# Performance work log

Measured on AMD Instinct MI355X. Metric: run time of the kernel, lower is better.

Reference implementation:

```python
import jax, jax.numpy as jnp
import numpy as np

D = 64; T = 128; B = 64; R = 20; SEE = 10; H = 4; C = 4
N = 300000; P = 4000; K = 256


def setup_inputs() -> dict:
    key = jax.random.key(0)
    ks = jax.random.split(key, 24)
    g = lambda k, s: jax.random.normal(k, s, dtype=jnp.float32) * 0.05
    return {
        "prob_id": jax.random.randint(ks[0], (T, B), 0, P),
        "skills": jax.random.randint(ks[1], (T, B, C), 0, K),
        "response": jax.random.randint(ks[2], (T, B), 0, 2),
        "bg_index": jax.random.randint(ks[3], (T, B, R), 0, N),
        "mem_prob_ids": jax.random.randint(ks[4], (N,), 0, P),
        "mem_resp": jax.random.randint(ks[5], (N,), 0, 2),
        "mem_concepts": jax.random.randint(ks[6], (N, C), 0, K),
        "states_mem": g(ks[7], (N, D)),
        "concept_emb": g(ks[8], (K - 1, D)),
        "prob_emb": g(ks[9], (P - 1, D)),
        "W_pred": g(ks[10], (9 * D, 1)), "b_pred": jnp.zeros((1,), jnp.float32),
        "W_ih": g(ks[11], (4 * D, 3 * D)), "W_hh": g(ks[12], (D, 3 * D)),
        "b_ih": jnp.zeros((3 * D,), jnp.float32), "b_hh": jnp.zeros((3 * D,), jnp.float32),
        "W_batch": g(ks[13], (H, 3 * D, D)), "b_batch": jnp.zeros((H, D), jnp.float32),
        "W_bg": g(ks[14], (H, 3 * D, D)), "b_bg": jnp.zeros((H, D), jnp.float32),
        "W_bgint": g(ks[15], (6 * D, 6 * D)), "b_bgint": jnp.zeros((6 * D,), jnp.float32),
        "W_hisint": g(ks[16], (2 * D, 6 * D)), "b_hisint": jnp.zeros((6 * D,), jnp.float32),
        "W_inmap": g(ks[17], (10 * D, 4 * D)), "b_inmap": jnp.zeros((4 * D,), jnp.float32),
        "dir_w": g(ks[18], (2, 1)), "heads_map": g(ks[19], (H, 1)),
    }


def _forward(floats, ints):
    (states_mem, concept_emb, prob_emb, W_pred, b_pred, W_ih, W_hh, b_ih, b_hh,
     W_batch, b_batch, W_bg, b_bg, W_bgint, b_bgint, W_hisint, b_hisint,
     W_inmap, b_inmap, dir_w, heads_map) = floats
    prob_id, skills, response, bg_index, mem_prob_ids, mem_resp, mem_concepts = ints
    f32 = states_mem.dtype
    # embedding tables with zero row 0 (padding id)
    prob_cat = jnp.concatenate([jnp.zeros((1, D), f32), prob_emb], axis=0)
    conc_cat = jnp.concatenate([jnp.zeros((1, D), f32), concept_emb], axis=0)

    def prob_rep(pid, sk):
        pr = prob_cat[pid]                                     # [..., D]
        fsum = jnp.sum((sk != 0).astype(f32), axis=-1)
        div = jnp.where(fsum == 0, 1.0, fsum)[..., None]
        mean = jnp.sum(conc_cat[sk], axis=-2) / div            # masked-mean concept emb
        return jnp.concatenate([mean, pr], axis=-1)            # [..., 2D]

    dw = jax.nn.softmax(dir_w, axis=0)                          # [2,1]
    hm = heads_map[:, 0]                                        # [H]

    def step(carry, xt):
        h, h_buf, resp_buf, v_buf, t = carry
        pid, sk, resp, bgi = xt
        respf = resp.astype(f32)
        v = prob_rep(pid, sk)                                   # [B,2D]
        hidden_v = jnp.concatenate([h, v], axis=-1)             # [B,3D]
        bgi = bgi[:, :SEE]                                      # keep first see_ref refs
        bg_h = states_mem[bgi]                                  # [B,S,D] irregular gather
        bg_v = prob_rep(mem_prob_ids[bgi], mem_concepts[bgi])   # [B,S,2D]
        bg_r = mem_resp[bgi].astype(f32)[..., None]             # [B,S,1]
        all_hv = jnp.concatenate([bg_h, bg_v], axis=-1)         # [B,S,3D]
        bg_ctx = jnp.concatenate([all_hv * bg_r, all_hv * (1.0 - bg_r)], axis=-1)  # [B,S,6D]
        # multi-head attention over retrieved background states
        q = jnp.einsum('bk,hkd->bhd', hidden_v, W_batch) + b_batch[None]
        kk = jnp.einsum('bsk,hkd->bhsd', all_hv, W_bg) + b_bg[None, :, None, :]
        att = jax.nn.softmax(jnp.einsum('bhd,bhsd->bhs', q, kk) / np.sqrt(3.0 * D), axis=-1)
        heads = jnp.einsum('bhs,bsk->bhk', att, bg_ctx)          # [B,H,6D]
        bg_atts = jnp.einsum('bhk,h->bk', heads, hm)             # [B,6D]
        # attention over own history (positions 0..t valid)
        rb = resp_buf.astype(f32)[..., None]                     # [B,T+1,1]
        hr_cat = jnp.concatenate([h_buf * rb, h_buf * (1.0 - rb)], axis=-1)  # [B,T+1,2D]
        sc = jnp.einsum('bk,btk->bt', v, v_buf) / np.sqrt(2.0 * D)
        sc = jnp.where(jnp.arange(T + 1)[None, :] <= t, sc, -1e9)
        his_atts = jnp.einsum('bt,btk->bk', jax.nn.softmax(sc, axis=-1), hr_cat)  # [B,2D]
        peer = (bg_atts @ W_bgint + b_bgint) * dw[0, 0] + (his_atts @ W_hisint + b_hisint) * dw[1, 0]
        prob = (jnp.concatenate([peer, v, h], axis=-1) @ W_pred + b_pred)[:, 0]
        v_resp = jnp.concatenate([v * respf[:, None], v * (1.0 - respf[:, None])], axis=-1)
        gru_in = jnp.concatenate([peer, v_resp], axis=-1) @ W_inmap + b_inmap  # [B,4D]
        # GRU cell (torch GRUCell convention)
        gx = gru_in @ W_ih + b_ih
        gh = h @ W_hh + b_hh
        xr, xz, xn = jnp.split(gx, 3, axis=-1)
        hr, hz, hn = jnp.split(gh, 3, axis=-1)
        r = jax.nn.sigmoid(xr + hr)
        z = jax.nn.sigmoid(xz + hz)
        n = jnp.tanh(xn + r * hn)
        new_h = (1.0 - z) * n + z * h
        h_buf = h_buf.at[:, t + 1].set(new_h)
        resp_buf = resp_buf.at[:, t + 1].set(resp.astype(resp_buf.dtype))
        v_buf = v_buf.at[:, t + 1].set(v)
        return (new_h, h_buf, resp_buf, v_buf, t + 1), prob

    init = (jnp.zeros((B, D), f32), jnp.zeros((B, T + 1, D), f32),
            jnp.zeros((B, T + 1), jnp.int32), jnp.zeros((B, T + 1, 2 * D), f32),
            jnp.int32(0))
    xs = (prob_id, skills, response.astype(jnp.int32), bg_index)
    _, probs = jax.lax.scan(step, init, xs)                      # [T,B]
    return probs.T.reshape(-1)                                   # concat over batch, seq_num=T


def reference(prob_id, skills, response, bg_index, mem_prob_ids, mem_resp, mem_concepts,
              states_mem, concept_emb, prob_emb, W_pred, b_pred, W_ih, W_hh, b_ih, b_hh,
              W_batch, b_batch, W_bg, b_bg, W_bgint, b_bgint, W_hisint, b_hisint,
              W_inmap, b_inmap, dir_w, heads_map):
    floats = (states_mem, concept_emb, prob_emb, W_pred, b_pred, W_ih, W_hh, b_ih, b_hh,
              W_batch, b_batch, W_bg, b_bg, W_bgint, b_bgint, W_hisint, b_hisint,
              W_inmap, b_inmap, dir_w, heads_map)
    ints = (prob_id, skills, response, bg_index, mem_prob_ids, mem_resp, mem_concepts)
    return _forward(floats, ints)
```

## Files before the change

### kernel.cpp

```cpp
#include <hip/hip_runtime.h>
#include <hip/hip_bf16.h>

#define TT 128
#define BB 64
#define NITEM (TT*BB*SEE)
#define SEE 10
typedef __attribute__((ext_vector_type(8))) short short8;
typedef __attribute__((ext_vector_type(4))) float floatx4;

static __device__ __forceinline__ float wave_sum(float v) {
  v += __shfl_xor(v, 32); v += __shfl_xor(v, 16); v += __shfl_xor(v, 8);
  v += __shfl_xor(v, 4);  v += __shfl_xor(v, 2);  v += __shfl_xor(v, 1);
  return v;
}
static __device__ __forceinline__ float wave_max(float v) {
  v = fmaxf(v, __shfl_xor(v, 32)); v = fmaxf(v, __shfl_xor(v, 16)); v = fmaxf(v, __shfl_xor(v, 8));
  v = fmaxf(v, __shfl_xor(v, 4));  v = fmaxf(v, __shfl_xor(v, 2));  v = fmaxf(v, __shfl_xor(v, 1));
  return v;
}
static __device__ __forceinline__ unsigned short f2bf(float x) {
  __hip_bfloat16 h = __float2bfloat16(x);
  return *reinterpret_cast<unsigned short*>(&h);
}
static __device__ __forceinline__ float bf2f(unsigned short u) {
  unsigned v = ((unsigned)u) << 16;
  return __builtin_bit_cast(float, v);
}
static __device__ __forceinline__ unsigned int pack2(float lo, float hi) {
  return (unsigned int)f2bf(lo) | ((unsigned int)f2bf(hi) << 16);
}
static __device__ __forceinline__ void ldsbar() {
  asm volatile("s_waitcnt lgkmcnt(0)" ::: "memory");
  __builtin_amdgcn_s_barrier();
  asm volatile("" ::: "memory");
}

__global__ void build_v(const int* __restrict__ prob_id, const int* __restrict__ skills,
                        const float* __restrict__ concept_emb, const float* __restrict__ prob_emb,
                        float* __restrict__ V, float* __restrict__ VT) {
  int tb = blockIdx.x; int t = tb >> 6, b = tb & 63; int d = threadIdx.x;
  int pid = prob_id[tb];
  float pr = pid ? prob_emb[(pid - 1) * 64 + d] : 0.0f;
  int cnt = 0; float sum = 0.0f;
#pragma unroll
  for (int c = 0; c < 4; ++c) {
    int sk = skills[tb * 4 + c];
    if (sk) { ++cnt; sum += concept_emb[(sk - 1) * 64 + d]; }
  }
  float mean = sum / (float)(cnt ? cnt : 1);
  V[tb * 128 + d] = mean;
  V[tb * 128 + 64 + d] = pr;
  VT[b * 16384 + d * 128 + t] = mean;
  VT[b * 16384 + (64 + d) * 128 + t] = pr;
}

__global__ __launch_bounds__(256) void gather_ahv(
    const int* __restrict__ bg_index, const int* __restrict__ mem_prob_ids,
    const int* __restrict__ mem_concepts, const float* __restrict__ states_mem,
    const float* __restrict__ concept_emb, const float* __restrict__ prob_emb,
    unsigned short* __restrict__ AHV) {
  int gid = blockIdx.x * 256 + threadIdx.x;
  int item = gid / 96, c2 = gid - 96 * item; int d = 2 * c2;
  int t = item / 640; int rem = item - t * 640; int b = rem / 10; int s = rem - b * 10;
  int g = bg_index[(t * 64 + b) * 20 + s];
  float v0, v1;
  if (d < 64) {
    float2 sv = *(const float2*)&states_mem[g * 64 + d];
    v0 = sv.x; v1 = sv.y;
  } else if (d < 128) {
    int dd = d - 64; float s0 = 0.f, s1 = 0.f; int cnt = 0;
#pragma unroll
    for (int c = 0; c < 4; ++c) {
      int sk = mem_concepts[g * 4 + c];
      if (sk) { ++cnt; float2 e = *(const float2*)&concept_emb[(sk - 1) * 64 + dd]; s0 += e.x; s1 += e.y; }
    }
    float inv = 1.0f / (float)(cnt ? cnt : 1);
    v0 = s0 * inv; v1 = s1 * inv;
  } else {
    int dd = d - 128; int pid = mem_prob_ids[g];
    if (pid) { float2 pv = *(const float2*)&prob_emb[(pid - 1) * 64 + dd]; v0 = pv.x; v1 = pv.y; }
    else { v0 = 0.f; v1 = 0.f; }
  }
  *(unsigned int*)&AHV[(size_t)item * 192 + d] = pack2(v0, v1);
}

__global__ __launch_bounds__(256) void gemm_f32(
    const float* __restrict__ A, const float* __restrict__ B, float* __restrict__ C,
    const float* __restrict__ bias, int M, int N, int K,
    int lda, int ldb, int ldc, long sA, long sB, long sC, float scale) {
  __shared__ __align__(16) float As[64 * 36];
  __shared__ __align__(16) float Bs[32 * 64];
  const float* Ab = A + (long)blockIdx.z * sA;
  const float* Bb = B + (long)blockIdx.z * sB;
  float* Cb = C + (long)blockIdx.z * sC;
  int m0 = blockIdx.y * 64, n0 = blockIdx.x * 64;
  int tid = threadIdx.x;
  int ti = tid & 15, tj = tid >> 4;
  float acc[4][4] = {};
  for (int kc = 0; kc < K; kc += 32) {
#pragma unroll
    for (int p = 0; p < 2; ++p) {
      int q = tid + 256 * p;
      int row = q >> 3, kq = q & 7;
      *(float4*)&As[row * 36 + 4 * kq] = *(const float4*)&Ab[(size_t)(m0 + row) * lda + kc + 4 * kq];
    }
#pragma unroll
    for (int p = 0; p < 2; ++p) {
      int q = tid + 256 * p;
      int k = q >> 4, nq = q & 15;
      *(float4*)&Bs[k * 64 + 4 * nq] = *(const float4*)&Bb[(size_t)(kc + k) * ldb + n0 + 4 * nq];
    }
    __syncthreads();
#pragma unroll
    for (int k4 = 0; k4 < 8; ++k4) {
      float4 av[4], bv[4];
#pragma unroll
      for (int m = 0; m < 4; ++m) av[m] = *(const float4*)&As[(ti + 16 * m) * 36 + 4 * k4];
#pragma unroll
      for (int kk = 0; kk < 4; ++kk) bv[kk] = *(const float4*)&Bs[(4 * k4 + kk) * 64 + 4 * tj];
#pragma unroll
      for (int m = 0; m < 4; ++m) {
        const float* ap = (const float*)&av[m];
#pragma unroll
        for (int kk = 0; kk < 4; ++kk) {
          float a = ap[kk];
          acc[m][0] += a * bv[kk].x; acc[m][1] += a * bv[kk].y;
          acc[m][2] += a * bv[kk].z; acc[m][3] += a * bv[kk].w;
        }
      }
    }
    __syncthreads();
  }
  float4 bq = make_float4(0.f, 0.f, 0.f, 0.f);
  if (bias) bq = *(const float4*)&bias[n0 + 4 * tj];
#pragma unroll
  for (int m = 0; m < 4; ++m) {
    int row = m0 + ti + 16 * m;
    float4 o;
    o.x = acc[m][0] * scale + bq.x; o.y = acc[m][1] * scale + bq.y;
    o.z = acc[m][2] * scale + bq.z; o.w = acc[m][3] * scale + bq.w;
    *(float4*)&Cb[(size_t)row * ldc + n0 + 4 * tj] = o;
  }
}

__global__ __launch_bounds__(256) void k_small(
    const float* __restrict__ W_batch, const float* __restrict__ W_bg, const float* __restrict__ b_bg,
    const float* __restrict__ W_bgint, const float* __restrict__ b_bgint,
    const float* __restrict__ W_hisint, const float* __restrict__ b_hisint,
    const float* __restrict__ W_ih, const float* __restrict__ b_ih, const float* __restrict__ b_inmap,
    const float* __restrict__ W_pred, const float* __restrict__ b_pred, const float* __restrict__ dir_w,
    const float* __restrict__ b_batch,
    const float* __restrict__ M12, unsigned short* __restrict__ B1T, float* __restrict__ Hmix,
    float* __restrict__ WgT, float* __restrict__ BQG, float* __restrict__ biasQG,
    float* __restrict__ c4, float* __restrict__ cgx, float* __restrict__ uh,
    float* __restrict__ bgp, float* __restrict__ c0, float* __restrict__ dwv) {
  int idx = blockIdx.x * 256 + threadIdx.x;
  const int R0 = 49152, R1 = 86016, R2 = 122880, R3 = 147456, R4 = 196608,
            R5 = 229376, R6 = 278528, R7 = 278784, R8 = 278976, R9 = 279104,
            R10 = 279488, R11 = 279489, R12 = 279491, R13 = 280131;
  if (idx < R0) {
    int k = idx >> 8, n = idx & 255; int h = n >> 6, i = n & 63;
    float s = 0.f;
    for (int d = 0; d < 64; ++d) s += W_bg[h * 12288 + k * 64 + d] * W_batch[h * 12288 + i * 64 + d];
    B1T[n * 192 + k] = f2bf(s);
  } else if (idx < R1) {
    int r = idx - R0; int k = r / 192, c = r - k * 192;
    float s = 0.f;
    for (int j = 0; j < 384; ++j) s += W_bgint[k * 384 + j] * M12[j * 192 + c];
    B1T[(256 + c) * 192 + k] = f2bf(s);
  } else if (idx < R2) {
    int r = idx - R1; int k = r / 192, c = r - k * 192;
    float s = 0.f;
    for (int j = 0; j < 384; ++j) s += W_bgint[(192 + k) * 384 + j] * M12[j * 192 + c];
    B1T[(448 + c) * 192 + k] = f2bf(s);
  } else if (idx < R3) {
    int r = idx - R2; int i = r / 192, c = r - i * 192;
    float s = 0.f;
    for (int j = 0; j < 384; ++j) s += W_hisint[i * 384 + j] * M12[j * 192 + c];
    Hmix[i * 192 + c] = s;
  } else if (idx < R4) {
    int r = idx - R3; int h = r / 12288; int rem = r - h * 12288; int d = rem / 192, k = rem - d * 192;
    WgT[r] = W_bg[h * 12288 + k * 64 + d];
  } else if (idx < R5) {
    int r = idx - R4; int i = r >> 8, n = r & 255; int h = n >> 6, d = n & 63;
    BQG[i * 640 + n] = W_batch[h * 12288 + (64 + i) * 64 + d];
  } else if (idx < R6) {
    int r = idx - R5; int i = r / 384, c = r - i * 384;
    BQG[i * 640 + 256 + c] = (c < 192) ? M12[(384 + i) * 192 + c] : M12[(512 + i) * 192 + (c - 192)];
  } else if (idx < R7) {
    int n = idx - R6; int h = n >> 6, i = n & 63;
    float s = 0.f;
    for (int d = 0; d < 64; ++d) s += W_batch[h * 12288 + i * 64 + d] * b_bg[h * 64 + d];
    c4[n] = s;
  } else if (idx < R8) {
    int c = idx - R7;
    float e0 = __expf(dir_w[0]), e1 = __expf(dir_w[1]);
    float dw0 = e0 / (e0 + e1), dw1 = e1 / (e0 + e1);
    float s = b_ih[c];
    for (int i = 0; i < 256; ++i) s += b_inmap[i] * W_ih[i * 192 + c];
    for (int k = 0; k < 384; ++k) s += (dw0 * b_bgint[k] + dw1 * b_hisint[k]) * M12[k * 192 + c];
    cgx[c] = s;
  } else if (idx < R9) {
    int i = idx - R8;
    float s = 0.f;
    for (int j = 0; j < 384; ++j) s += W_hisint[i * 384 + j] * W_pred[j];
    uh[i] = s;
  } else if (idx < R10) {
    int k = idx - R9;
    float s = 0.f;
    for (int j = 0; j < 384; ++j) s += W_bgint[k * 384 + j] * W_pred[j];
    bgp[k] = s;
  } else if (idx < R11) {
    float e0 = __expf(dir_w[0]), e1 = __expf(dir_w[1]);
    float dw0 = e0 / (e0 + e1), dw1 = e1 / (e0 + e1);
    float s = b_pred[0];
    for (int k = 0; k < 384; ++k) s += (dw0 * b_bgint[k] + dw1 * b_hisint[k]) * W_pred[k];
    c0[0] = s;
  } else if (idx < R12) {
    float e0 = __expf(dir_w[0]), e1 = __expf(dir_w[1]);
    dwv[idx - R11] = (idx == R11) ? e0 / (e0 + e1) : e1 / (e0 + e1);
  } else if (idx < R13) {
    int i = idx - R12;
    biasQG[i] = (i < 256) ? b_batch[i] : 0.f;
  }
}

#define APAD 200
#define BPAD 40
__global__ __launch_bounds__(256) void big_gemm(
    const int* __restrict__ bg_index, const int* __restrict__ mem_resp,
    const unsigned short* __restrict__ AHV, const unsigned short* __restrict__ B1T,
    const float* __restrict__ c4, unsigned short* __restrict__ P4s16, float* __restrict__ Cg) {
  __shared__ unsigned short As[128 * APAD];
  __shared__ unsigned short Bs[128 * BPAD];
  __shared__ int rf_l[128];
  int mt = blockIdx.x;
  int tid = threadIdx.x;
  int lane = tid & 63, wv = tid >> 6;
  if (tid < 128) {
    int item = mt * 128 + tid;
    int t = item / 640; int rem = item - t * 640; int b = rem / 10; int s = rem - b * 10;
    int g = bg_index[(t * 64 + b) * 20 + s];
    rf_l[tid] = mem_resp[g];
  }
  for (int i = tid; i < 128 * 24; i += 256) {
    int row = i / 24, c = i - 24 * row;
    *(float4*)&As[row * APAD + c * 8] = *(const float4*)&AHV[(size_t)(mt * 128 + row) * 192 + c * 8];
  }
  int l15 = lane & 15, q = lane >> 4;
  int mh = (wv & 1) * 64, nh = (wv >> 1) * 64;
  const float invs192 = 0.07216878364870323f;
  for (int nt = 0; nt < 5; ++nt) {
    int n0 = nt * 128;
    floatx4 acc[4][4];
#pragma unroll
    for (int mi = 0; mi < 4; ++mi)
#pragma unroll
      for (int ni = 0; ni < 4; ++ni)
#pragma unroll
        for (int r = 0; r < 4; ++r) acc[mi][ni][r] = 0.f;
    for (int kc = 0; kc < 6; ++kc) {
      __syncthreads();
#pragma unroll
      for (int u = 0; u < 2; ++u) {
        int un = tid * 2 + u;
        int n = un >> 2, kk = (un & 3) * 8;
        *(float4*)&Bs[n * BPAD + kk] = *(const float4*)&B1T[(size_t)(n0 + n) * 192 + kc * 32 + kk];
      }
      __syncthreads();
      short8 a[4], bfr[4];
#pragma unroll
      for (int mi = 0; mi < 4; ++mi)
        a[mi] = *reinterpret_cast<const short8*>(&As[(mh + mi * 16 + l15) * APAD + kc * 32 + q * 8]);
#pragma unroll
      for (int ni = 0; ni < 4; ++ni)
        bfr[ni] = *reinterpret_cast<const short8*>(&Bs[(nh + ni * 16 + l15) * BPAD + q * 8]);
#pragma unroll
      for (int mi = 0; mi < 4; ++mi)
#pragma unroll
        for (int ni = 0; ni < 4; ++ni)
          acc[mi][ni] = __builtin_amdgcn_mfma_f32_16x16x32_bf16(a[mi], bfr[ni], acc[mi][ni], 0, 0, 0);
    }
    float c4v[4];
    if (n0 + nh < 256) {
#pragma unroll
      for (int ni = 0; ni < 4; ++ni) c4v[ni] = c4[n0 + nh + ni * 16 + l15];
    }
#pragma unroll
    for (int mi = 0; mi < 4; ++mi) {
#pragma unroll
      for (int r = 0; r < 4; ++r) {
        int row = mh + mi * 16 + q * 4 + r;
        int item = mt * 128 + row;
        int rf = rf_l[row];
#pragma unroll
        for (int ni = 0; ni < 4; ++ni) {
          int coln = n0 + nh + ni * 16 + l15;
          float o = acc[mi][ni][r];
          if (coln < 256) {
            P4s16[(size_t)item * 256 + coln] = f2bf((o + c4v[ni]) * invs192);
          } else if (coln < 448) {
            if (rf) Cg[(size_t)item * 192 + (coln - 256)] = o;
          } else {
            if (!rf) Cg[(size_t)item * 192 + (coln - 448)] = o;
          }
        }
      }
    }
  }
}

__global__ __launch_bounds__(256) void k5(
    const int* __restrict__ bg_index, const int* __restrict__ mem_resp,
    const unsigned short* __restrict__ AHV, const float* __restrict__ RQ,
    const float* __restrict__ QVG, const float* __restrict__ b_bg,
    const float* __restrict__ bgp, const float* __restrict__ V,
    const float* __restrict__ W_pred, const float* __restrict__ c0,
    float* __restrict__ SQVb, float* __restrict__ cbp, float* __restrict__ PROBC) {
  int tb = blockIdx.x;
  int tid = threadIdx.x;
  int lane = tid & 63, wv = tid >> 6;
  __shared__ float ahv[10 * 196];
  __shared__ float rql[4 * 196];
  __shared__ float bgpl[384];
  __shared__ int rf_s[10];
  __shared__ float cqb[4];
  if (tid < 10) { int g = bg_index[tb * 20 + tid]; rf_s[tid] = mem_resp[g]; }
  for (int i = tid; i < 384; i += 256) bgpl[i] = bgp[i];
  for (int i = tid; i < 768; i += 256) { int h = i / 192, c = i - h * 192; rql[h * 196 + c] = RQ[(size_t)tb * 768 + i]; }
  {
    const unsigned short* AH = &AHV[(size_t)tb * 10 * 192];
    for (int i = tid; i < 1920; i += 256) {
      int s = i / 192, c = i - 192 * s;
      ahv[s * 196 + c] = bf2f(AH[s * 192 + c]);
    }
  }
  if (tid < 4) {
    float s = 0.f;
    for (int d = 0; d < 64; ++d) s += QVG[(size_t)tb * 640 + tid * 64 + d] * b_bg[tid * 64 + d];
    cqb[tid] = s;
  }
  __syncthreads();
  const float invs192 = 0.07216878364870323f;
  for (int q = 0; q < 10; ++q) {
    float v = ahv[q * 196 + lane] * rql[wv * 196 + lane]
            + ahv[q * 196 + 64 + lane] * rql[wv * 196 + 64 + lane]
            + ahv[q * 196 + 128 + lane] * rql[wv * 196 + 128 + lane];
    v = wave_sum(v);
    if (lane == 0) SQVb[tb * 40 + wv * 10 + q] = (v + cqb[wv]) * invs192;
  }
  if (wv == 0) {
    for (int q = 0; q < 10; ++q) {
      int off = rf_s[q] ? 0 : 192;
      float v = ahv[q * 196 + lane] * bgpl[off + lane]
              + ahv[q * 196 + 64 + lane] * bgpl[off + 64 + lane]
              + ahv[q * 196 + 128 + lane] * bgpl[off + 128 + lane];
      v = wave_sum(v);
      if (lane == 0) cbp[tb * 10 + q] = v;
    }
  }
  if (wv == 1) {
    float v = V[tb * 128 + lane] * W_pred[384 + lane] + V[tb * 128 + 64 + lane] * W_pred[448 + lane];
    v = wave_sum(v);
    if (lane == 0) PROBC[tb] = v + c0[0];
  }
}

__global__ __launch_bounds__(64) void prep_pw(const float* S, const int* response,
                                              float* PW, float* PR) {
  int bt = blockIdx.x; int b = bt >> 7, t = bt & 127;
  int lane = threadIdx.x;
  size_t row = (size_t)bt * 128;
  float s0 = (lane == 0) ? 0.f : ((lane <= t) ? S[row + lane - 1] : -1e30f);
  float s1 = (lane + 64 <= t) ? S[row + lane + 63] : -1e30f;
  float m = wave_max(fmaxf(s0, s1));
  float e0 = (lane <= t) ? __expf(s0 - m) : 0.f;
  float e1 = (lane + 64 <= t) ? __expf(s1 - m) : 0.f;
  float inv = 1.f / wave_sum(e0 + e1);
  float r0 = (lane >= 1) ? (float)response[(lane - 1) * 64 + b] : 0.f;
  float r1 = (float)response[(lane + 63) * 64 + b];
  PW[row + lane] = e0 * inv;
  PW[row + 64 + lane] = e1 * inv;
  PR[row + lane] = e0 * inv * r0;
  PR[row + 64 + lane] = e1 * inv * r1;
}

__global__ __launch_bounds__(512) void seq_kernel(
    const int* __restrict__ response, const unsigned short* __restrict__ P4s16,
    const float* __restrict__ SQVb, const float* __restrict__ Cg,
    const float* __restrict__ QVG, const float* __restrict__ cbp,
    const float* __restrict__ PROBC, const float* __restrict__ PW,
    const float* __restrict__ PR, const float* __restrict__ Hmix,
    const float* __restrict__ W_hh, const float* __restrict__ b_hh,
    const float* __restrict__ cgx, const float* __restrict__ uh,
    const float* __restrict__ W_pred, const float* __restrict__ heads_map,
    const float* __restrict__ dwv, float* __restrict__ out) {
  int b = blockIdx.x;
  int tid = threadIdx.x;
  int lane = tid & 63, wv = tid >> 6;
  int cg3 = lane * 3;
  float hreg[16][3], wreg[8][3];
#pragma unroll
  for (int ii = 0; ii < 16; ++ii)
#pragma unroll
    for (int cc = 0; cc < 3; ++cc) hreg[ii][cc] = Hmix[(wv * 16 + ii) * 192 + cg3 + cc];
#pragma unroll
  for (int ii = 0; ii < 8; ++ii)
#pragma unroll
    for (int cc = 0; cc < 3; ++cc) wreg[ii][cc] = W_hh[(wv * 8 + ii) * 192 + cg3 + cc];
  float wph_reg[8], uh_reg[16];
  if (lane == 0) {
#pragma unroll
    for (int j = 0; j < 8; ++j) wph_reg[j] = W_pred[512 + wv * 8 + j];
#pragma unroll
    for (int ii = 0; ii < 16; ++ii) uh_reg[ii] = uh[wv * 16 + ii];
  }
  float bhh_reg = 0.f;
  if (tid >= 64 && tid < 256) bhh_reg = b_hh[tid - 64];
  float cgx0 = 0.f, cgx1 = 0.f, cgx2 = 0.f;
  if (tid < 64) { cgx0 = cgx[tid]; cgx1 = cgx[64 + tid]; cgx2 = cgx[128 + tid]; }
  float hmr = 0.f;
  if (tid >= 448 && tid < 452) hmr = heads_map[tid - 448];

  __shared__ float h_hist[128][64];
  __shared__ __align__(16) float PWl[128];
  __shared__ __align__(16) float PRl[128];
  __shared__ __align__(16) float h_cur[64];
  __shared__ float part_sc[8][40];
  __shared__ __align__(16) float e_l[40];
  __shared__ __align__(16) float inv_l[4];
  __shared__ __align__(16) float hisA[128];
  __shared__ float red8[8][128];
  __shared__ float redWg[8][192];
  __shared__ float redWh[8][192];
  __shared__ float gh_l[192];
  __shared__ float hwp_p[8], phis_p[8];
  __shared__ int resp_l[128];

  for (int i = tid; i < 128 * 64; i += 512) ((float*)h_hist)[i] = 0.f;
  if (tid < 64) h_cur[tid] = 0.f;
  if (tid >= 256 && tid < 384) resp_l[tid - 256] = response[(tid - 256) * 64 + b];
  float dw0 = dwv[0], dw1 = dwv[1];

  int sc_off = 0;
  if (lane < 40) { int hh = lane / 10, s = lane - hh * 10; sc_off = s * 256 + hh * 64 + wv * 8; }
  short8 pf8 = {};
  if (lane < 40) pf8 = *(const short8*)&P4s16[(size_t)b * 2560 + sc_off];
  float pf_sqv = 0.f;
  if (tid >= 384 && tid < 424) pf_sqv = SQVb[b * 40 + (tid - 384)];
  float pf_cg0[10], pf_cg1[10], pf_cg2[10];
  float pf_gxA0 = 0.f, pf_gxA1 = 0.f, pf_gxA2 = 0.f, pf_gxB0 = 0.f, pf_gxB1 = 0.f, pf_gxB2 = 0.f;
  if (tid < 64) {
#pragma unroll
    for (int s = 0; s < 10; ++s) {
      size_t base = (size_t)(b * 10 + s) * 192;
      pf_cg0[s] = Cg[base + tid]; pf_cg1[s] = Cg[base + 64 + tid]; pf_cg2[s] = Cg[base + 128 + tid];
    }
    size_t gb = (size_t)b * 640 + 256;
    pf_gxA0 = QVG[gb + tid]; pf_gxA1 = QVG[gb + 64 + tid]; pf_gxA2 = QVG[gb + 128 + tid];
    pf_gxB0 = QVG[gb + 192 + tid]; pf_gxB1 = QVG[gb + 256 + tid]; pf_gxB2 = QVG[gb + 320 + tid];
  }
  float pf_cbp[10]; float pf_probc = 0.f;
  if (tid == 448) {
#pragma unroll
    for (int s = 0; s < 10; ++s) pf_cbp[s] = cbp[b * 10 + s];
    pf_probc = PROBC[b];
  }
  float4 pf_pw = make_float4(0, 0, 0, 0), pf_pr = pf_pw;
  if (tid >= 128 && tid < 160) pf_pw = *(const float4*)&PW[((size_t)(b * 128 + 0)) * 128 + 4 * (tid - 128)];
  else if (tid >= 160 && tid < 192) pf_pr = *(const float4*)&PR[((size_t)(b * 128 + 0)) * 128 + 4 * (tid - 160)];
  if (tid >= 128 && tid < 160) *(float4*)&PWl[4 * (tid - 128)] = pf_pw;
  else if (tid >= 160 && tid < 192) *(float4*)&PRl[4 * (tid - 160)] = pf_pr;
  if (tid >= 128 && tid < 160) pf_pw = *(const float4*)&PW[((size_t)(b * 128 + 1)) * 128 + 4 * (tid - 128)];
  else if (tid >= 160 && tid < 192) pf_pr = *(const float4*)&PR[((size_t)(b * 128 + 1)) * 128 + 4 * (tid - 160)];
  ldsbar();

  for (int t = 0; t < 128; ++t) {
    int tn = (t < 127) ? t + 1 : 127;
    int tbn = tn * 64 + b;
    float4 ha = *(const float4*)&h_cur[wv * 8];
    float4 hb = *(const float4*)&h_cur[wv * 8 + 4];
    if (lane < 40) {
      const unsigned short* pp = (const unsigned short*)&pf8;
      float v = ha.x * bf2f(pp[0]) + ha.y * bf2f(pp[1]) + ha.z * bf2f(pp[2]) + ha.w * bf2f(pp[3])
              + hb.x * bf2f(pp[4]) + hb.y * bf2f(pp[5]) + hb.z * bf2f(pp[6]) + hb.w * bf2f(pp[7]);
      part_sc[wv][lane] = v;
      pf8 = *(const short8*)&P4s16[(size_t)tbn * 2560 + sc_off];
    }
    {
      float hl[8] = {ha.x, ha.y, ha.z, ha.w, hb.x, hb.y, hb.z, hb.w};
      float l0 = 0.f, l1 = 0.f, l2 = 0.f;
#pragma unroll
      for (int ii = 0; ii < 8; ++ii) {
        l0 += hl[ii] * wreg[ii][0]; l1 += hl[ii] * wreg[ii][1]; l2 += hl[ii] * wreg[ii][2];
      }
      redWg[wv][cg3] = l0; redWg[wv][cg3 + 1] = l1; redWg[wv][cg3 + 2] = l2;
      if (lane == 0) {
        float hp = 0.f;
#pragma unroll
        for (int j = 0; j < 8; ++j) hp += hl[j] * wph_reg[j];
        hwp_p[wv] = hp;
      }
    }
    {
      int j0 = wv * 16;
      float aR = 0.f, aA = 0.f;
#pragma unroll
      for (int k = 0; k < 16; ++k) {
        float hv = h_hist[j0 + k][lane];
        aA += PWl[j0 + k] * hv; aR += PRl[j0 + k] * hv;
      }
      red8[wv][lane] = aR; red8[wv][64 + lane] = aA;
    }
    ldsbar();
    if (tid < 64) {
      float sR = 0.f, sA = 0.f;
#pragma unroll
      for (int g = 0; g < 8; ++g) { sR += red8[g][tid]; sA += red8[g][64 + tid]; }
      hisA[tid] = sR; hisA[64 + tid] = sA - sR;
    } else if (tid < 256) {
      int c = tid - 64; float g = 0.f;
#pragma unroll
      for (int gg = 0; gg < 8; ++gg) g += redWg[gg][c];
      gh_l[c] = g + bhh_reg;
    } else if (tid >= 384 && tid < 424) {
      int p = tid - 384;
      float s = pf_sqv;
#pragma unroll
      for (int w = 0; w < 8; ++w) s += part_sc[w][p];
      e_l[p] = __expf(s);
      pf_sqv = SQVb[tbn * 40 + p];
    }
    ldsbar();
    {
      float4 h0 = *(const float4*)&hisA[wv * 16];
      float4 h1 = *(const float4*)&hisA[wv * 16 + 4];
      float4 h2 = *(const float4*)&hisA[wv * 16 + 8];
      float4 h3 = *(const float4*)&hisA[wv * 16 + 12];
      float hA[16] = {h0.x, h0.y, h0.z, h0.w, h1.x, h1.y, h1.z, h1.w,
                      h2.x, h2.y, h2.z, h2.w, h3.x, h3.y, h3.z, h3.w};
      float l0 = 0.f, l1 = 0.f, l2 = 0.f;
#pragma unroll
      for (int ii = 0; ii < 16; ++ii) {
        l0 += hA[ii] * hreg[ii][0]; l1 += hA[ii] * hreg[ii][1]; l2 += hA[ii] * hreg[ii][2];
      }
      redWh[wv][cg3] = l0; redWh[wv][cg3 + 1] = l1; redWh[wv][cg3 + 2] = l2;
      if (lane == 0) {
        float pp = 0.f;
#pragma unroll
        for (int ii = 0; ii < 16; ++ii) pp += hA[ii] * uh_reg[ii];
        phis_p[wv] = pp;
      }
    }
    if (tid >= 448 && tid < 452) {
      int h = tid - 448;
      float den = 0.f;
#pragma unroll
      for (int s = 0; s < 10; ++s) den += e_l[h * 10 + s];
      inv_l[h] = hmr / den;
    }
    ldsbar();
    if (tid < 64 || tid == 448) {
      float4 iv = *(const float4*)&inv_l[0];
      float ev[40];
#pragma unroll
      for (int qq = 0; qq < 10; ++qq) *(float4*)&ev[4 * qq] = *(const float4*)&e_l[4 * qq];
      float ws[10];
#pragma unroll
      for (int s = 0; s < 10; ++s)
        ws[s] = iv.x * ev[s] + iv.y * ev[10 + s] + iv.z * ev[20 + s] + iv.w * ev[30 + s];
      if (tid < 64) {
        float gxh0 = 0.f, gxh1 = 0.f, gxh2 = 0.f;
#pragma unroll
        for (int g = 0; g < 8; ++g) {
          gxh0 += redWh[g][tid]; gxh1 += redWh[g][64 + tid]; gxh2 += redWh[g][128 + tid];
        }
        float gbg0 = 0.f, gbg1 = 0.f, gbg2 = 0.f;
#pragma unroll
        for (int s = 0; s < 10; ++s) {
          gbg0 += ws[s] * pf_cg0[s]; gbg1 += ws[s] * pf_cg1[s]; gbg2 += ws[s] * pf_cg2[s];
        }
        int rn = resp_l[t];
        float xr = dw0 * gbg0 + dw1 * gxh0 + (rn ? pf_gxA0 : pf_gxB0) + cgx0;
        float xz = dw0 * gbg1 + dw1 * gxh1 + (rn ? pf_gxA1 : pf_gxB1) + cgx1;
        float xn = dw0 * gbg2 + dw1 * gxh2 + (rn ? pf_gxA2 : pf_gxB2) + cgx2;
        float hr = gh_l[tid], hz = gh_l[64 + tid], hn = gh_l[128 + tid];
        float r = 1.f / (1.f + __expf(-(xr + hr)));
        float z = 1.f / (1.f + __expf(-(xz + hz)));
        float n = tanhf(xn + r * hn);
        float hnew = (1.f - z) * n + z * h_cur[tid];
        h_cur[tid] = hnew;
        if (t < 127) h_hist[t + 1][tid] = hnew;
#pragma unroll
        for (int s = 0; s < 10; ++s) {
          size_t base = (size_t)(tbn * 10 + s) * 192;
          pf_cg0[s] = Cg[base + tid]; pf_cg1[s] = Cg[base + 64 + tid]; pf_cg2[s] = Cg[base + 128 + tid];
        }
        size_t gb = (size_t)tbn * 640 + 256;
        pf_gxA0 = QVG[gb + tid]; pf_gxA1 = QVG[gb + 64 + tid]; pf_gxA2 = QVG[gb + 128 + tid];
        pf_gxB0 = QVG[gb + 192 + tid]; pf_gxB1 = QVG[gb + 256 + tid]; pf_gxB2 = QVG[gb + 320 + tid];
      } else {
        float pbg = 0.f;
#pragma unroll
        for (int s = 0; s < 10; ++s) pbg += ws[s] * pf_cbp[s];
        float ph = 0.f, hw = 0.f;
#pragma unroll
        for (int g = 0; g < 8; ++g) { ph += phis_p[g]; hw += hwp_p[g]; }
        out[b * 128 + t] = dw0 * pbg + dw1 * ph + hw + pf_probc;
#pragma unroll
        for (int s = 0; s < 10; ++s) pf_cbp[s] = cbp[tbn * 10 + s];
        pf_probc = PROBC[tbn];
      }
    } else if (tid >= 128 && tid < 192) {
      if (tid < 160) *(float4*)&PWl[4 * (tid - 128)] = pf_pw;
      else *(float4*)&PRl[4 * (tid - 160)] = pf_pr;
      int rn2 = (t + 2 < 128) ? t + 2 : 127;
      if (tid < 160) pf_pw = *(const float4*)&PW[((size_t)(b * 128 + rn2)) * 128 + 4 * (tid - 128)];
      else pf_pr = *(const float4*)&PR[((size_t)(b * 128 + rn2)) * 128 + 4 * (tid - 160)];
    }
    ldsbar();
  }
}

extern "C" void kernel_launch(void* const* d_in, const int* in_sizes, int n_in,
                              void* d_out, int out_size, void* d_ws, size_t ws_size,
                              hipStream_t stream) {
  const int* prob_id      = (const int*)d_in[0];
  const int* skills       = (const int*)d_in[1];
  const int* response     = (const int*)d_in[2];
  const int* bg_index     = (const int*)d_in[3];
  const int* mem_prob_ids = (const int*)d_in[4];
  const int* mem_resp     = (const int*)d_in[5];
  const int* mem_concepts = (const int*)d_in[6];
  const float* states_mem  = (const float*)d_in[7];
  const float* concept_emb = (const float*)d_in[8];
  const float* prob_emb    = (const float*)d_in[9];
  const float* W_pred   = (const float*)d_in[10];
  const float* b_pred   = (const float*)d_in[11];
  const float* W_ih     = (const float*)d_in[12];
  const float* W_hh     = (const float*)d_in[13];
  const float* b_ih     = (const float*)d_in[14];
  const float* b_hh     = (const float*)d_in[15];
  const float* W_batch  = (const float*)d_in[16];
  const float* b_batch  = (const float*)d_in[17];
  const float* W_bg     = (const float*)d_in[18];
  const float* b_bg     = (const float*)d_in[19];
  const float* W_bgint  = (const float*)d_in[20];
  const float* b_bgint  = (const float*)d_in[21];
  const float* W_hisint = (const float*)d_in[22];
  const float* b_hisint = (const float*)d_in[23];
  const float* W_inmap  = (const float*)d_in[24];
  const float* b_inmap  = (const float*)d_in[25];
  const float* dir_w    = (const float*)d_in[26];
  const float* heads_map= (const float*)d_in[27];
  float* out = (float*)d_out;

  float* w = (float*)d_ws;
  size_t off = 0;
  auto alloc = [&](size_t n) { float* p = w + off; off += (n + 3) & ~(size_t)3; return p; };
  float* M12    = alloc(640 * 192);
  unsigned short* B1T = (unsigned short*)alloc(640 * 192 / 2);
  float* Hmix   = alloc(128 * 192);
  float* WgT    = alloc(4 * 192 * 64);
  float* BQG    = alloc(128 * 640);
  float* biasQG = alloc(640);
  float* c4     = alloc(256);
  float* cgx    = alloc(192);
  float* uh     = alloc(128);
  float* bgp    = alloc(384);
  float* c0     = alloc(1);
  float* dwv    = alloc(2);
  float* V      = alloc((size_t)8192 * 128);
  float* VT     = alloc((size_t)64 * 128 * 128);
  float* QVG    = alloc((size_t)8192 * 640);
  float* RQ     = alloc((size_t)8192 * 768);
  float* S      = alloc((size_t)64 * 128 * 128);
  float* PR     = alloc((size_t)64 * 128 * 128);
  unsigned short* AHV = (unsigned short*)alloc((size_t)NITEM * 192 / 2);
  unsigned short* P4s16 = (unsigned short*)alloc((size_t)NITEM * 256 / 2);
  float* Cg     = alloc((size_t)NITEM * 192);
  float* SQVb   = alloc((size_t)8192 * 40);
  float* cbp    = alloc((size_t)NITEM);
  float* PROBC  = alloc(8192);
  (void)ws_size; (void)in_sizes; (void)n_in; (void)out_size;

  build_v<<<8192, 64, 0, stream>>>(prob_id, skills, concept_emb, prob_emb, V, VT);
  gather_ahv<<<NITEM * 96 / 256, 256, 0, stream>>>(bg_index, mem_prob_ids, mem_concepts,
      states_mem, concept_emb, prob_emb, AHV);
  gemm_f32<<<dim3(3, 10, 1), 256, 0, stream>>>(W_inmap, W_ih, M12, nullptr,
      640, 192, 256, 256, 192, 192, 0, 0, 0, 1.0f);
  k_small<<<1095, 256, 0, stream>>>(W_batch, W_bg, b_bg, W_bgint, b_bgint, W_hisint, b_hisint,
      W_ih, b_ih, b_inmap, W_pred, b_pred, dir_w, b_batch, M12, B1T, Hmix, WgT, BQG, biasQG,
      c4, cgx, uh, bgp, c0, dwv);
  gemm_f32<<<dim3(10, 128, 1), 256, 0, stream>>>(V, BQG, QVG, biasQG,
      8192, 640, 128, 128, 640, 640, 0, 0, 0, 1.0f);
  gemm_f32<<<dim3(3, 128, 4), 256, 0, stream>>>(QVG, WgT, RQ, nullptr,
      8192, 192, 64, 640, 192, 768, 64, 12288, 192, 1.0f);
  gemm_f32<<<dim3(2, 2, 64), 256, 0, stream>>>(V, VT, S, nullptr,
      128, 128, 128, 8192, 128, 128, 128, 16384, 16384, 0.08838834764831845f);
  prep_pw<<<8192, 64, 0, stream>>>(S, response, S, PR);
  big_gemm<<<dim3(640), 256, 0, stream>>>(bg_index, mem_resp, AHV, B1T, c4, P4s16, Cg);
  k5<<<8192, 256, 0, stream>>>(bg_index, mem_resp, AHV, RQ, QVG, b_bg, bgp, V, W_pred, c0,
      SQVb, cbp, PROBC);
  seq_kernel<<<64, 512, 0, stream>>>(response, P4s16, SQVb, Cg, QVG, cbp, PROBC,
      S, PR, Hmix, W_hh, b_hh, cgx, uh, W_pred, heads_map, dwv, out);
}
```

Before: 762.9 us.

## Fold QVG and RQ GEMMs into one bf16 MFMA GEMM with precomposed weights

Precomposes the W_batch·W_bg product (with its bias) on device so that RQ can be computed directly from V. The two chained fp32 GEMMs (V→QVG, QVG→RQ) become a single bf16 MFMA GEMM producing a combined 1408-wide QVR buffer. This removes one launch and the intermediate round trip, and moves the work onto matrix cores. In exchange it adds bf16 rounding to the QVG and RQ values and a larger k_small prep kernel.

Measured after the change: 751.7 us. No clear change (-1.5%).

```diff
diff --git a/kernel.cpp b/kernel.cpp
--- a/kernel.cpp
+++ b/kernel.cpp
@@ -37,7 +37,8 @@
 
 __global__ void build_v(const int* __restrict__ prob_id, const int* __restrict__ skills,
                         const float* __restrict__ concept_emb, const float* __restrict__ prob_emb,
-                        float* __restrict__ V, float* __restrict__ VT) {
+                        float* __restrict__ V, float* __restrict__ VT,
+                        unsigned short* __restrict__ V16) {
   int tb = blockIdx.x; int t = tb >> 6, b = tb & 63; int d = threadIdx.x;
   int pid = prob_id[tb];
   float pr = pid ? prob_emb[(pid - 1) * 64 + d] : 0.0f;
@@ -50,6 +51,8 @@
   float mean = sum / (float)(cnt ? cnt : 1);
   V[tb * 128 + d] = mean;
   V[tb * 128 + 64 + d] = pr;
+  V16[tb * 128 + d] = f2bf(mean);
+  V16[tb * 128 + 64 + d] = f2bf(pr);
   VT[b * 16384 + d * 128 + t] = mean;
   VT[b * 16384 + (64 + d) * 128 + t] = pr;
 }
@@ -151,13 +154,13 @@
     const float* __restrict__ W_pred, const float* __restrict__ b_pred, const float* __restrict__ dir_w,
     const float* __restrict__ b_batch,
     const float* __restrict__ M12, unsigned short* __restrict__ B1T, float* __restrict__ Hmix,
-    float* __restrict__ WgT, float* __restrict__ BQG, float* __restrict__ biasQG,
+    unsigned short* __restrict__ BRQT, float* __restrict__ bias_all,
     float* __restrict__ c4, float* __restrict__ cgx, float* __restrict__ uh,
     float* __restrict__ bgp, float* __restrict__ c0, float* __restrict__ dwv) {
   int idx = blockIdx.x * 256 + threadIdx.x;
-  const int R0 = 49152, R1 = 86016, R2 = 122880, R3 = 147456, R4 = 196608,
-            R5 = 229376, R6 = 278528, R7 = 278784, R8 = 278976, R9 = 279104,
-            R10 = 279488, R11 = 279489, R12 = 279491, R13 = 280131;
+  const int R0 = 49152, R1 = 86016, R2 = 122880, R3 = 147456, R4 = 180224,
+            R5 = 229376, R6 = 327680, R7 = 327936, R8 = 328128, R9 = 328256,
+            R10 = 328640, R11 = 328641, R12 = 328643, R13 = 330051;
   if (idx < R0) {
     int k = idx >> 8, n = idx & 255; int h = n >> 6, i = n & 63;
     float s = 0.f;
@@ -179,14 +182,17 @@
     for (int j = 0; j < 384; ++j) s += W_hisint[i * 384 + j] * M12[j * 192 + c];
     Hmix[i * 192 + c] = s;
   } else if (idx < R4) {
-    int r = idx - R3; int h = r / 12288; int rem = r - h * 12288; int d = rem / 192, k = rem - d * 192;
-    WgT[r] = W_bg[h * 12288 + k * 64 + d];
+    int r = idx - R3; int n = r >> 7, j = r & 127; int h = n >> 6, d = n & 63;
+    BRQT[n * 128 + j] = f2bf(W_batch[h * 12288 + (64 + j) * 64 + d]);
   } else if (idx < R5) {
-    int r = idx - R4; int i = r >> 8, n = r & 255; int h = n >> 6, d = n & 63;
-    BQG[i * 640 + n] = W_batch[h * 12288 + (64 + i) * 64 + d];
+    int r = idx - R4; int c = r >> 7, j = r & 127;
+    float v = (c < 192) ? M12[(384 + j) * 192 + c] : M12[(512 + j) * 192 + (c - 192)];
+    BRQT[(256 + c) * 128 + j] = f2bf(v);
   } else if (idx < R6) {
-    int r = idx - R5; int i = r / 384, c = r - i * 384;
-    BQG[i * 640 + 256 + c] = (c < 192) ? M12[(384 + i) * 192 + c] : M12[(512 + i) * 192 + (c - 192)];
+    int r = idx - R5; int n = r >> 7, j = r & 127; int h = n / 192, k = n - h * 192;
+    float s = 0.f;
+    for (int d = 0; d < 64; ++d) s += W_batch[h * 12288 + (64 + j) * 64 + d] * W_bg[h * 12288 + k * 64 + d];
+    BRQT[(640 + n) * 128 + j] = f2bf(s);
   } else if (idx < R7) {
     int n = idx - R6; int h = n >> 6, i = n & 63;
     float s = 0.f;
@@ -221,12 +227,83 @@
     dwv[idx - R11] = (idx == R11) ? e0 / (e0 + e1) : e1 / (e0 + e1);
   } else if (idx < R13) {
     int i = idx - R12;
-    biasQG[i] = (i < 256) ? b_batch[i] : 0.f;
+    float v = 0.f;
+    if (i < 256) v = b_batch[i];
+    else if (i >= 640) {
+      int n = i - 640; int h = n / 192, k = n - h * 192;
+      float s = 0.f;
+      for (int d = 0; d < 64; ++d) s += b_batch[h * 64 + d] * W_bg[h * 12288 + k * 64 + d];
+      v = s;
+    }
+    bias_all[i] = v;
+  }
+}
+
+#define VPAD 136
+#define BPAD 40
+__global__ __launch_bounds__(256) void mfma_qvr(
+    const unsigned short* __restrict__ V16, const unsigned short* __restrict__ BRQT,
+    const float* __restrict__ bias_all, float* __restrict__ QVR) {
+  __shared__ unsigned short As[128 * VPAD];
+  __shared__ unsigned short Bs[128 * BPAD];
+  int mt = blockIdx.x, ntt = blockIdx.y;
+  int n0 = ntt * 128;
+  int tid = threadIdx.x;
+  int lane = tid & 63, wv = tid >> 6;
+  for (int i = tid; i < 128 * 16; i += 256) {
+    int row = i >> 4, c = i & 15;
+    *(float4*)&As[row * VPAD + c * 8] = *(const float4*)&V16[(size_t)(mt * 128 + row) * 128 + c * 8];
+  }
+  int l15 = lane & 15, q = lane >> 4;
+  int mh = (wv & 1) * 64, nh = (wv >> 1) * 64;
+  floatx4 acc[4][4];
+#pragma unroll
+  for (int mi = 0; mi < 4; ++mi)
+#pragma unroll
+    for (int ni = 0; ni < 4; ++ni)
+#pragma unroll
+      for (int r = 0; r < 4; ++r) acc[mi][ni][r] = 0.f;
+  for (int kc = 0; kc < 4; ++kc) {
+    __syncthreads();
+#pragma unroll
+    for (int u = 0; u < 2; ++u) {
+      int un = tid * 2 + u;
+      int n = un >> 2, kk = (un & 3) * 8;
+      *(float4*)&Bs[n * BPAD + kk] = *(const float4*)&BRQT[(size_t)(n0 + n) * 128 + kc * 32 + kk];
+    }
+    __syncthreads();
+    short8 a[4], bfr[4];
+#pragma unroll
+    for (int mi = 0; mi < 4; ++mi)
+      a[mi] = *reinterpret_cast<const short8*>(&As[(mh + mi * 16 + l15) * VPAD + kc * 32 + q * 8]);
+#pragma unroll
+    for (int ni = 0; ni < 4; ++ni)
+      bfr[ni] = *reinterpret_cast<const short8*>(&Bs[(nh + ni * 16 + l15) * BPAD + q * 8]);
+#pragma unroll
+    for (int mi = 0; mi < 4; ++mi)
+#pragma unroll
+      for (int ni = 0; ni < 4; ++ni)
+        acc[mi][ni] = __builtin_amdgcn_mfma_f32_16x16x32_bf16(a[mi], bfr[ni], acc[mi][ni], 0, 0, 0);
+  }
+  float bv[4];
+#pragma unroll
+  for (int ni = 0; ni < 4; ++ni) bv[ni] = bias_all[n0 + nh + ni * 16 + l15];
+#pragma unroll
+  for (int mi = 0; mi < 4; ++mi) {
+#pragma unroll
+    for (int r = 0; r < 4; ++r) {
+      int row = mh + mi * 16 + q * 4 + r;
+      size_t item = (size_t)(mt * 128 + row);
+#pragma unroll
+      for (int ni = 0; ni < 4; ++ni) {
+        int coln = n0 + nh + ni * 16 + l15;
+        QVR[item * 1408 + coln] = acc[mi][ni][r] + bv[ni];
+      }
+    }
   }
 }
 
 #define APAD 200
-#define BPAD 40
 __global__ __launch_bounds__(256) void big_gemm(
     const int* __restrict__ bg_index, const int* __restrict__ mem_resp,
     const unsigned short* __restrict__ AHV, const unsigned short* __restrict__ B1T,
@@ -312,9 +389,8 @@
 
 __global__ __launch_bounds__(256) void k5(
     const int* __restrict__ bg_index, const int* __restrict__ mem_resp,
-    const unsigned short* __restrict__ AHV, const float* __restrict__ RQ,
-    const float* __restrict__ QVG, const float* __restrict__ b_bg,
-    const float* __restrict__ bgp, const float* __restrict__ V,
+    const unsigned short* __restrict__ AHV, const float* __restrict__ QVR,
+    const float* __restrict__ b_bg, const float* __restrict__ bgp, const float* __restrict__ V,
     const float* __restrict__ W_pred, const float* __restrict__ c0,
     float* __restrict__ SQVb, float* __restrict__ cbp, float* __restrict__ PROBC) {
   int tb = blockIdx.x;
@@ -327,7 +403,7 @@
   __shared__ float cqb[4];
   if (tid < 10) { int g = bg_index[tb * 20 + tid]; rf_s[tid] = mem_resp[g]; }
   for (int i = tid; i < 384; i += 256) bgpl[i] = bgp[i];
-  for (int i = tid; i < 768; i += 256) { int h = i / 192, c = i - h * 192; rql[h * 196 + c] = RQ[(size_t)tb * 768 + i]; }
+  for (int i = tid; i < 768; i += 256) { int h = i / 192, c = i - h * 192; rql[h * 196 + c] = QVR[(size_t)tb * 1408 + 640 + i]; }
   {
     const unsigned short* AH = &AHV[(size_t)tb * 10 * 192];
     for (int i = tid; i < 1920; i += 256) {
@@ -337,7 +413,7 @@
   }
   if (tid < 4) {
     float s = 0.f;
-    for (int d = 0; d < 64; ++d) s += QVG[(size_t)tb * 640 + tid * 64 + d] * b_bg[tid * 64 + d];
+    for (int d = 0; d < 64; ++d) s += QVR[(size_t)tb * 1408 + tid * 64 + d] * b_bg[tid * 64 + d];
     cqb[tid] = s;
   }
   __syncthreads();
@@ -388,7 +464,7 @@
 __global__ __launch_bounds__(512) void seq_kernel(
     const int* __restrict__ response, const unsigned short* __restrict__ P4s16,
     const float* __restrict__ SQVb, const float* __restrict__ Cg,
-    const float* __restrict__ QVG, const float* __restrict__ cbp,
+    const float* __restrict__ QVR, const float* __restrict__ cbp,
     const float* __restrict__ PROBC, const float* __restrict__ PW,
     const float* __restrict__ PR, const float* __restrict__ Hmix,
     const float* __restrict__ W_hh, const float* __restrict__ b_hh,
@@ -456,9 +532,9 @@
       size_t base = (size_t)(b * 10 + s) * 192;
       pf_cg0[s] = Cg[base + tid]; pf_cg1[s] = Cg[base + 64 + tid]; pf_cg2[s] = Cg[base + 128 + tid];
     }
-    size_t gb = (size_t)b * 640 + 256;
-    pf_gxA0 = QVG[gb + tid]; pf_gxA1 = QVG[gb + 64 + tid]; pf_gxA2 = QVG[gb + 128 + tid];
-    pf_gxB0 = QVG[gb + 192 + tid]; pf_gxB1 = QVG[gb + 256 + tid]; pf_gxB2 = QVG[gb + 320 + tid];
+    size_t gb = (size_t)b * 1408 + 256;
+    pf_gxA0 = QVR[gb + tid]; pf_gxA1 = QVR[gb + 64 + tid]; pf_gxA2 = QVR[gb + 128 + tid];
+    pf_gxB0 = QVR[gb + 192 + tid]; pf_gxB1 = QVR[gb + 256 + tid]; pf_gxB2 = QVR[gb + 320 + tid];
   }
   float pf_cbp[10]; float pf_probc = 0.f;
   if (tid == 448) {
@@ -596,9 +672,9 @@
           size_t base = (size_t)(tbn * 10 + s) * 192;
           pf_cg0[s] = Cg[base + tid]; pf_cg1[s] = Cg[base + 64 + tid]; pf_cg2[s] = Cg[base + 128 + tid];
         }
-        size_t gb = (size_t)tbn * 640 + 256;
-        pf_gxA0 = QVG[gb + tid]; pf_gxA1 = QVG[gb + 64 + tid]; pf_gxA2 = QVG[gb + 128 + tid];
-        pf_gxB0 = QVG[gb + 192 + tid]; pf_gxB1 = QVG[gb + 256 + tid]; pf_gxB2 = QVG[gb + 320 + tid];
+        size_t gb = (size_t)tbn * 1408 + 256;
+        pf_gxA0 = QVR[gb + tid]; pf_gxA1 = QVR[gb + 64 + tid]; pf_gxA2 = QVR[gb + 128 + tid];
+        pf_gxB0 = QVR[gb + 192 + tid]; pf_gxB1 = QVR[gb + 256 + tid]; pf_gxB2 = QVR[gb + 320 + tid];
       } else {
         float pbg = 0.f;
 #pragma unroll
@@ -661,9 +737,8 @@
   float* M12    = alloc(640 * 192);
   unsigned short* B1T = (unsigned short*)alloc(640 * 192 / 2);
   float* Hmix   = alloc(128 * 192);
-  float* WgT    = alloc(4 * 192 * 64);
-  float* BQG    = alloc(128 * 640);
-  float* biasQG = alloc(640);
+  unsigned short* BRQT = (unsigned short*)alloc(1408 * 128 / 2);
+  float* bias_all = alloc(1408);
   float* c4     = alloc(256);
   float* cgx    = alloc(192);
   float* uh     = alloc(128);
@@ -671,9 +746,9 @@
   float* c0     = alloc(1);
   float* dwv    = alloc(2);
   float* V      = alloc((size_t)8192 * 128);
+  unsigned short* V16 = (unsigned short*)alloc((size_t)8192 * 128 / 2);
   float* VT     = alloc((size_t)64 * 128 * 128);
-  float* QVG    = alloc((size_t)8192 * 640);
-  float* RQ     = alloc((size_t)8192 * 768);
+  float* QVR    = alloc((size_t)8192 * 1408);
   float* S      = alloc((size_t)64 * 128 * 128);
   float* PR     = alloc((size_t)64 * 128 * 128);
   unsigned short* AHV = (unsigned short*)alloc((size_t)NITEM * 192 / 2);
@@ -684,24 +759,21 @@
   float* PROBC  = alloc(8192);
   (void)ws_size; (void)in_sizes; (void)n_in; (void)out_size;
 
-  build_v<<<8192, 64, 0, stream>>>(prob_id, skills, concept_emb, prob_emb, V, VT);
+  build_v<<<8192, 64, 0, stream>>>(prob_id, skills, concept_emb, prob_emb, V, VT, V16);
+  gemm_f32<<<dim3(3, 10, 1), 256, 0, stream>>>(W_inmap, W_ih, M12, nullptr,
+      640, 192, 256, 256, 192, 192, 0, 0, 0, 1.0f);
+  k_small<<<1290, 256, 0, stream>>>(W_batch, W_bg, b_bg, W_bgint, b_bgint, W_hisint, b_hisint,
+      W_ih, b_ih, b_inmap, W_pred, b_pred, dir_w, b_batch, M12, B1T, Hmix, BRQT, bias_all,
+      c4, cgx, uh, bgp, c0, dwv);
   gather_ahv<<<NITEM * 96 / 256, 256, 0, stream>>>(bg_index, mem_prob_ids, mem_concepts,
       states_mem, concept_emb, prob_emb, AHV);
-  gemm_f32<<<dim3(3, 10, 1), 256, 0, stream>>>(W_inmap, W_ih, M12, nullptr,
-      640, 192, 256, 256, 192, 192, 0, 0, 0, 1.0f);
-  k_small<<<1095, 256, 0, stream>>>(W_batch, W_bg, b_bg, W_bgint, b_bgint, W_hisint, b_hisint,
-      W_ih, b_ih, b_inmap, W_pred, b_pred, dir_w, b_batch, M12, B1T, Hmix, WgT, BQG, biasQG,
-      c4, cgx, uh, bgp, c0, dwv);
-  gemm_f32<<<dim3(10, 128, 1), 256, 0, stream>>>(V, BQG, QVG, biasQG,
-      8192, 640, 128, 128, 640, 640, 0, 0, 0, 1.0f);
-  gemm_f32<<<dim3(3, 128, 4), 256, 0, stream>>>(QVG, WgT, RQ, nullptr,
-      8192, 192, 64, 640, 192, 768, 64, 12288, 192, 1.0f);
+  mfma_qvr<<<dim3(64, 11), 256, 0, stream>>>(V16, BRQT, bias_all, QVR);
   gemm_f32<<<dim3(2, 2, 64), 256, 0, stream>>>(V, VT, S, nullptr,
       128, 128, 128, 8192, 128, 128, 128, 16384, 16384, 0.08838834764831845f);
   prep_pw<<<8192, 64, 0, stream>>>(S, response, S, PR);
   big_gemm<<<dim3(640), 256, 0, stream>>>(bg_index, mem_resp, AHV, B1T, c4, P4s16, Cg);
-  k5<<<8192, 256, 0, stream>>>(bg_index, mem_resp, AHV, RQ, QVG, b_bg, bgp, V, W_pred, c0,
+  k5<<<8192, 256, 0, stream>>>(bg_index, mem_resp, AHV, QVR, b_bg, bgp, V, W_pred, c0,
       SQVb, cbp, PROBC);
-  seq_kernel<<<64, 512, 0, stream>>>(response, P4s16, SQVb, Cg, QVG, cbp, PROBC,
+  seq_kernel<<<64, 512, 0, stream>>>(response, P4s16, SQVb, Cg, QVR, cbp, PROBC,
       S, PR, Hmix, W_hh, b_hh, cgx, uh, W_pred, heads_map, dwv, out);
 }
```
